# Kernel tuning notes

Hardware: AMD Instinct MI355X
Metric: run time of the kernel (lower is better)

Reference implementation:

```python
import jax, jax.numpy as jnp
import numpy as np

N, NDIM, K, M = 65536, 512, 512, 200


def setup_inputs() -> dict:
    key = jax.random.key(0)
    k1, k2, k3, k4, k5 = jax.random.split(key, 5)
    data = jax.random.normal(k1, (N, NDIM), dtype=jnp.float32)
    # Orthogonal projection A, as in __init__: QR of randn with sign fix
    A0 = np.asarray(jax.random.normal(k2, (NDIM, K), dtype=jnp.float32), dtype=np.float64)
    Q, R = np.linalg.qr(A0)
    A = jnp.asarray(Q * np.sign(np.diag(R)), dtype=jnp.float32)
    # Monotonic knot grids on roughly [-4, 4] with M knots per direction
    span = 8.0 / (M - 1)
    dx = jax.random.uniform(k3, (K, M - 1), minval=0.5 * span, maxval=1.5 * span)
    xx = jnp.concatenate([jnp.full((K, 1), -4.0), -4.0 + jnp.cumsum(dx, axis=1)], axis=1).astype(jnp.float32)
    dy = jax.random.uniform(k4, (K, M - 1), minval=0.5 * span, maxval=1.5 * span)
    yy = jnp.concatenate([jnp.full((K, 1), -4.0), -4.0 + jnp.cumsum(dy, axis=1)], axis=1).astype(jnp.float32)
    delta = jax.random.uniform(k5, (K, M), minval=0.5, maxval=2.0, dtype=jnp.float32)
    return {"data": data, "A": A, "xx": xx, "yy": yy, "delta": delta}


def _rq_spline_forward(x, xx, yy, delta):
    """Monotonic rational-quadratic spline, applied per dimension.
    x: (N, K) values; xx, yy, delta: (K, M) knot positions / values / derivatives.
    Returns (y, log|dy/dx|), both (N, K).
    """
    Mk = xx.shape[1]
    # Per-dimension bin search: idx in [0, Mk]
    idx = jax.vmap(jnp.searchsorted, in_axes=(0, 1))(xx, x).T  # (N, K)
    below = idx == 0
    above = idx == Mk
    b = jnp.clip(idx, 1, Mk - 1) - 1  # interior bin index, (N, K)
    bt = b.T  # (K, N) for take_along_axis on (K, M) tables
    g = lambda t, o: jnp.take_along_axis(t, bt + o, axis=1).T  # -> (N, K)
    xk, xk1 = g(xx, 0), g(xx, 1)
    yk, yk1 = g(yy, 0), g(yy, 1)
    dk, dk1 = g(delta, 0), g(delta, 1)
    dx = xk1 - xk
    dy = yk1 - yk
    s = dy / dx  # bin slope
    xi = jnp.clip((x - xk) / dx, 0.0, 1.0)  # clipped so out-of-range pts stay finite
    xi1 = 1.0 - xi
    denom = s + (dk1 + dk - 2.0 * s) * xi * xi1
    y_in = yk + dy * (s * xi * xi + dk * xi * xi1) / denom
    logd_in = (2.0 * jnp.log(s)
               + jnp.log(dk1 * xi * xi + 2.0 * s * xi * xi1 + dk * xi1 * xi1)
               - 2.0 * jnp.log(denom))
    # Linear extrapolation outside the knot range with endpoint derivatives
    x0, xN_ = xx[:, 0], xx[:, -1]
    y0, yN_ = yy[:, 0], yy[:, -1]
    d0, dN_ = delta[:, 0], delta[:, -1]
    y = jnp.where(below, y0 + d0 * (x - x0),
                  jnp.where(above, yN_ + dN_ * (x - xN_), y_in))
    logd = jnp.where(below, jnp.log(d0),
                     jnp.where(above, jnp.log(dN_), logd_in))
    return y, logd


def reference(data, A, xx, yy, delta):
    data0 = data @ A                    # (N, K) sliced projection
    remaining = data - data0 @ A.T      # component orthogonal to the slices
    y, logd = _rq_spline_forward(data0, xx, yy, delta)
    logj = jnp.sum(logd, axis=1)        # (N,) log-Jacobian
    out = remaining + y @ A.T
    return out, logj
```

## Files before the change

kernel.cpp:

```cpp
#include <hip/hip_runtime.h>

#define N_ROWS 65536
#define DIM 512
#define MKNOTS 200
#define KT 16
#define NCELL 384
#define TILE 256
#define TPB 4

typedef _Float16 f16x8 __attribute__((ext_vector_type(8)));
typedef _Float16 f16x4 __attribute__((ext_vector_type(4)));
typedef float f32x4 __attribute__((ext_vector_type(4)));

__device__ inline void gload16(const void* g, void* l) {
  __builtin_amdgcn_global_load_lds(
      (const __attribute__((address_space(1))) void*)g,
      (__attribute__((address_space(3))) void*)l,
      16, 0, 0);
}

template <bool S3, bool ADDSRC>
__global__ __launch_bounds__(256)
void gemm_k(const _Float16* __restrict__ Ah, const _Float16* __restrict__ Al,
            const _Float16* __restrict__ Bth, const _Float16* __restrict__ Btl,
            const float* __restrict__ addsrc, float* __restrict__ C)
{
  __shared__ alignas(16) _Float16 smem[S3 ? 16384 : 8192];
  _Float16* sAh = smem;
  _Float16* sBh = smem + 4096;
  _Float16* sAl = S3 ? smem + 8192  : smem;
  _Float16* sBl = S3 ? smem + 12288 : smem;

  const int tid  = threadIdx.x;
  const int bm   = blockIdx.x * 128;
  const int bn   = blockIdx.y * 128;
  const int wm   = ((tid >> 6) >> 1) * 64;
  const int wn   = ((tid >> 6) & 1) * 64;
  const int lane = tid & 63;
  const int lm   = lane & 15;
  const int quad = lane >> 4;
  const int sr   = tid >> 2;
  const int sc   = (tid & 3) * 8;

  const _Float16* gAh = Ah  + (size_t)(bm + sr) * DIM + sc;
  const _Float16* gBh = Bth + (size_t)(bn + sr) * DIM + sc;
  const _Float16* gAl = S3 ? (Al  + (size_t)(bm + sr) * DIM + sc) : gAh;
  const _Float16* gBl = S3 ? (Btl + (size_t)(bn + sr) * DIM + sc) : gBh;

  f32x4 acc[4][4] = {};

  for (int k0 = 0; k0 < DIM; k0 += 32) {
    gload16(gAh + k0,               sAh + tid * 8);
    gload16(gAh + k0 + 64 * DIM,    sAh + 2048 + tid * 8);
    gload16(gBh + k0,               sBh + tid * 8);
    gload16(gBh + k0 + 64 * DIM,    sBh + 2048 + tid * 8);
    if constexpr (S3) {
      gload16(gAl + k0,             sAl + tid * 8);
      gload16(gAl + k0 + 64 * DIM,  sAl + 2048 + tid * 8);
      gload16(gBl + k0,             sBl + tid * 8);
      gload16(gBl + k0 + 64 * DIM,  sBl + 2048 + tid * 8);
    }
    __syncthreads();

    f16x8 a_h[4], b_h[4], a_l[4], b_l[4];
    #pragma unroll
    for (int i = 0; i < 4; ++i) {
      a_h[i] = *(const f16x8*)&sAh[(wm + i * 16 + lm) * 32 + quad * 8];
      b_h[i] = *(const f16x8*)&sBh[(wn + i * 16 + lm) * 32 + quad * 8];
      if constexpr (S3) {
        a_l[i] = *(const f16x8*)&sAl[(wm + i * 16 + lm) * 32 + quad * 8];
        b_l[i] = *(const f16x8*)&sBl[(wn + i * 16 + lm) * 32 + quad * 8];
      }
    }
    #pragma unroll
    for (int i = 0; i < 4; ++i)
      #pragma unroll
      for (int j = 0; j < 4; ++j) {
        acc[i][j] = __builtin_amdgcn_mfma_f32_16x16x32_f16(a_h[i], b_h[j], acc[i][j], 0, 0, 0);
        if constexpr (S3) {
          acc[i][j] = __builtin_amdgcn_mfma_f32_16x16x32_f16(a_h[i], b_l[j], acc[i][j], 0, 0, 0);
          acc[i][j] = __builtin_amdgcn_mfma_f32_16x16x32_f16(a_l[i], b_h[j], acc[i][j], 0, 0, 0);
        }
      }
    __syncthreads();
  }

  #pragma unroll
  for (int i = 0; i < 4; ++i)
    #pragma unroll
    for (int j = 0; j < 4; ++j)
      #pragma unroll
      for (int r = 0; r < 4; ++r) {
        const int row = bm + wm + i * 16 + quad * 4 + r;
        const int col = bn + wn + j * 16 + lm;
        const size_t idx = (size_t)row * DIM + col;
        float v = acc[i][j][r];
        if constexpr (ADDSRC) v += addsrc[idx];
        C[idx] = v;
      }
}

__global__ __launch_bounds__(256)
void conv_data_k(const float* __restrict__ in, _Float16* __restrict__ hi,
                 _Float16* __restrict__ lo)
{
  const size_t i = ((size_t)blockIdx.x * 256 + threadIdx.x) * 4;
  const float4 v = *reinterpret_cast<const float4*>(in + i);
  f16x4 h, l;
  h.x = (_Float16)v.x; l.x = (_Float16)(v.x - (float)h.x);
  h.y = (_Float16)v.y; l.y = (_Float16)(v.y - (float)h.y);
  h.z = (_Float16)v.z; l.z = (_Float16)(v.z - (float)h.z);
  h.w = (_Float16)v.w; l.w = (_Float16)(v.w - (float)h.w);
  *reinterpret_cast<f16x4*>(hi + i) = h;
  *reinterpret_cast<f16x4*>(lo + i) = l;
}

__global__ __launch_bounds__(256)
void conv_A_k(const float* __restrict__ A, _Float16* __restrict__ Ah,
              _Float16* __restrict__ Al, _Float16* __restrict__ ATh,
              _Float16* __restrict__ ATl)
{
  const int i = blockIdx.x * 256 + threadIdx.x;
  const int r = i >> 9, c = i & 511;
  const float v = A[i];
  const _Float16 h = (_Float16)v;
  const _Float16 l = (_Float16)(v - (float)h);
  Ah[i] = h; Al[i] = l;
  ATh[c * 512 + r] = h; ATl[c * 512 + r] = l;
}

__global__ __launch_bounds__(256)
void prep_k(const float* __restrict__ xx, const float* __restrict__ yy,
            const float* __restrict__ dd, float4* __restrict__ pkG,
            unsigned char* __restrict__ bucketG)
{
  __shared__ float xr[MKNOTS], yr[MKNOTS];
  const int k = blockIdx.x, tid = threadIdx.x;
  if (tid < MKNOTS) {
    xr[tid] = xx[k * MKNOTS + tid];
    yr[tid] = yy[k * MKNOTS + tid];
  }
  __syncthreads();
  if (tid < MKNOTS) {
    const float x0 = xr[tid], y0 = yr[tid], d0 = dd[k * MKNOTS + tid];
    float s = 0.f;
    if (tid < MKNOTS - 1) s = (yr[tid + 1] - y0) / (xr[tid + 1] - x0);
    pkG[k * MKNOTS + tid] = float4{x0, y0, d0, s};
  }
  for (int c = tid; c < NCELL; c += 256) {
    const float cl = -4.f + (float)c * 0.03125f;
    int lo = 0, hi = MKNOTS;
    while (lo < hi) { const int mid = (lo + hi) >> 1; if (xr[mid] <= cl) lo = mid + 1; else hi = mid; }
    bucketG[k * NCELL + c] = (unsigned char)lo;
  }
}

__global__ __launch_bounds__(256)
void spline_k(const float* __restrict__ data0, const float4* __restrict__ pkG,
              const unsigned char* __restrict__ bucketG,
              _Float16* __restrict__ zH, float* __restrict__ ppart)
{
  __shared__ float sX[KT * 201];
  __shared__ float sY[KT * 201];
  __shared__ _Float16 sD[KT * 201 + 2];
  __shared__ float xT[TILE * 17];

  const int kBase = blockIdx.x * KT;
  const int nBase = blockIdx.y * (TILE * TPB);
  const int tid = threadIdx.x;

  for (int i = tid; i < KT * MKNOTS; i += 256) {
    const int r = i / MKNOTS, c = i - r * MKNOTS;
    const float4 v = pkG[(kBase + r) * MKNOTS + c];
    sX[r * 201 + c] = v.x;
    sY[r * 201 + c] = v.y;
    sD[r * 201 + c] = (_Float16)v.z;
  }
  __syncthreads();

  for (int tile = 0; tile < TPB; ++tile) {
    const int n0 = nBase + tile * TILE;

    #pragma unroll
    for (int rr = 0; rr < 4; ++rr) {
      const int r = rr * 64 + (tid >> 2);
      const float4 v = *((const float4*)(data0 + (size_t)(n0 + r) * DIM + kBase) + (tid & 3));
      float* dst = &xT[r * 17 + (tid & 3) * 4];
      dst[0] = v.x; dst[1] = v.y; dst[2] = v.z; dst[3] = v.w;
    }
    __syncthreads();

    float acc = 0.f;
    float zprev = 0.f;
    #pragma unroll 4
    for (int j = 0; j < KT; ++j) {
      const float x = xT[tid * 17 + j];

      int c = (int)((x + 4.f) * 32.f);
      c = min(max(c, 0), NCELL - 1);
      const int cnt0 = (int)bucketG[(kBase + j) * NCELL + c];

      const int p = min(cnt0, MKNOTS - 2);
      const int q0 = p - 1;
      const float* rx = &sX[j * 201];
      const float xm = rx[q0], x0 = rx[q0 + 1], x1 = rx[q0 + 2], x2 = rx[q0 + 3];
      const int t2 = (x0 < x ? 1 : 0) + (x1 < x ? 1 : 0);
      const int idx = p + t2;
      const bool below = (x <= -4.f);
      const bool above = (idx >= MKNOTS);
      const int b = idx - 1;

      const float xk  = (t2 == 0) ? xm : ((t2 == 1) ? x0 : x1);
      const float xk1 = (t2 == 0) ? x0 : ((t2 == 1) ? x1 : x2);
      const float yk  = sY[j * 201 + b];
      const float yk1 = sY[j * 201 + b + 1];
      const float dk  = (float)sD[j * 201 + b];
      const float dk1 = (float)sD[j * 201 + b + 1];

      const float dxk = xk1 - xk;
      const float rdx = __builtin_amdgcn_rcpf(dxk);
      const float s   = (yk1 - yk) * rdx;
      float xi = (x - xk) * rdx;
      xi = fminf(fmaxf(xi, 0.f), 1.f);
      const float xi1 = 1.f - xi;
      const float g = xi * xi1;
      const float den = s + (dk1 + dk - 2.f * s) * g;
      const float rden = __builtin_amdgcn_rcpf(den);
      const float y_in = yk + s * dxk * (s * xi * xi + dk * g) * rden;
      const float dnum = dk1 * xi * xi + 2.f * s * g + dk * xi1 * xi1;
      const float ld_in = __logf(s * s * dnum * rden * rden);

      const bool edge = below || above;
      const float y  = edge ? (yk + dk * (x - xk)) : y_in;
      const float ld = edge ? __logf(dk) : ld_in;
      acc += ld;

      const float z = y - x;
      if (j & 1) {
        union { _Float16 h[2]; unsigned int u; } pk2;
        pk2.h[0] = (_Float16)zprev; pk2.h[1] = (_Float16)z;
        ((unsigned int*)xT)[tid * 17 + (j >> 1)] = pk2.u;
      } else {
        zprev = z;
      }
    }
    ppart[(size_t)blockIdx.x * N_ROWS + n0 + tid] = acc;
    __syncthreads();

    const int w = tid & 7;
    #pragma unroll
    for (int ri = 0; ri < 8; ++ri) {
      const int r = ri * 32 + (tid >> 3);
      const unsigned int zz = ((const unsigned int*)xT)[r * 17 + w];
      *(unsigned int*)(zH + (size_t)(n0 + r) * DIM + kBase + w * 2) = zz;
    }
    __syncthreads();
  }
}

__global__ __launch_bounds__(256)
void reduce_k(const float* __restrict__ ppart, float* __restrict__ logj)
{
  const int n = blockIdx.x * 256 + threadIdx.x;
  float a = 0.f;
  #pragma unroll
  for (int t = 0; t < 32; ++t) a += ppart[(size_t)t * N_ROWS + n];
  logj[n] = a;
}

extern "C" void kernel_launch(void* const* d_in, const int* in_sizes, int n_in,
                              void* d_out, int out_size, void* d_ws, size_t ws_size,
                              hipStream_t stream)
{
  const float* data  = (const float*)d_in[0];
  const float* A     = (const float*)d_in[1];
  const float* xx    = (const float*)d_in[2];
  const float* yy    = (const float*)d_in[3];
  const float* delta = (const float*)d_in[4];

  float* out  = (float*)d_out;
  float* logj = out + (size_t)N_ROWS * DIM;

  _Float16* dHi = (_Float16*)d_ws;
  _Float16* dLo = dHi + (size_t)N_ROWS * DIM;
  _Float16* Ah  = dLo + (size_t)N_ROWS * DIM;
  _Float16* Al  = Ah + 512 * 512;
  _Float16* ATh = Al + 512 * 512;
  _Float16* ATl = ATh + 512 * 512;
  float* data0  = (float*)(ATl + 512 * 512);
  _Float16* zH  = dHi;
  float4* pkG = (float4*)dLo;
  unsigned char* bucketG = (unsigned char*)(pkG + 512 * MKNOTS);
  float* ppart = (float*)(bucketG + 512 * NCELL);

  conv_A_k<<<1024, 256, 0, stream>>>(A, Ah, Al, ATh, ATl);
  conv_data_k<<<(N_ROWS * DIM) / (256 * 4), 256, 0, stream>>>(data, dHi, dLo);

  gemm_k<true, false><<<dim3(N_ROWS / 128, DIM / 128), 256, 0, stream>>>(
      dHi, dLo, ATh, ATl, nullptr, data0);

  prep_k<<<512, 256, 0, stream>>>(xx, yy, delta, pkG, bucketG);

  spline_k<<<dim3(DIM / KT, N_ROWS / (TILE * TPB)), 256, 0, stream>>>(
      data0, pkG, bucketG, zH, ppart);

  reduce_k<<<N_ROWS / 256, 256, 0, stream>>>(ppart, logj);

  gemm_k<false, true><<<dim3(N_ROWS / 128, DIM / 128), 256, 0, stream>>>(
      zH, nullptr, Ah, nullptr, data, out);
}
```

Baseline: 601.6 us.

## Restructure spline kernel: packed float4 knot table, finer buckets, register-staged rows

The spline kernel now holds each knot as a packed float4 (x, y, delta, 1/dx) in LDS and uses a finer bucket grid (768 cells, 8 dims per block). That cuts the bin search to a single comparison and replaces the per-bin divide with a precomputed reciprocal. Each thread reads its own row's 8 inputs straight from global memory with prefetch, and writes 16-byte z vectors directly, removing the LDS transpose and barriers. The trade-off is uncoalesced strided row access, more blocks, and more partial sums for reduce_k to combine. It also sets an occupancy hint of 5 waves.

```diff
diff --git a/kernel.cpp b/kernel.cpp
--- a/kernel.cpp
+++ b/kernel.cpp
@@ -3,14 +3,16 @@
 #define N_ROWS 65536
 #define DIM 512
 #define MKNOTS 200
-#define KT 16
-#define NCELL 384
+#define KT 8
+#define NCELL 768
 #define TILE 256
 #define TPB 4
+#define NKT (DIM / KT)
 
 typedef _Float16 f16x8 __attribute__((ext_vector_type(8)));
 typedef _Float16 f16x4 __attribute__((ext_vector_type(4)));
 typedef float f32x4 __attribute__((ext_vector_type(4)));
+typedef unsigned int u32x4 __attribute__((ext_vector_type(4)));
 
 __device__ inline void gload16(const void* g, void* l) {
   __builtin_amdgcn_global_load_lds(
@@ -134,36 +136,32 @@
             const float* __restrict__ dd, float4* __restrict__ pkG,
             unsigned char* __restrict__ bucketG)
 {
-  __shared__ float xr[MKNOTS], yr[MKNOTS];
+  __shared__ float xr[MKNOTS];
   const int k = blockIdx.x, tid = threadIdx.x;
-  if (tid < MKNOTS) {
-    xr[tid] = xx[k * MKNOTS + tid];
-    yr[tid] = yy[k * MKNOTS + tid];
-  }
+  if (tid < MKNOTS) xr[tid] = xx[k * MKNOTS + tid];
   __syncthreads();
   if (tid < MKNOTS) {
-    const float x0 = xr[tid], y0 = yr[tid], d0 = dd[k * MKNOTS + tid];
-    float s = 0.f;
-    if (tid < MKNOTS - 1) s = (yr[tid + 1] - y0) / (xr[tid + 1] - x0);
-    pkG[k * MKNOTS + tid] = float4{x0, y0, d0, s};
+    const float x0 = xr[tid];
+    const float y0 = yy[k * MKNOTS + tid];
+    const float d0 = dd[k * MKNOTS + tid];
+    float rdx = 0.f;
+    if (tid < MKNOTS - 1) rdx = 1.0f / (xr[tid + 1] - x0);
+    pkG[k * MKNOTS + tid] = float4{x0, y0, d0, rdx};
   }
   for (int c = tid; c < NCELL; c += 256) {
-    const float cl = -4.f + (float)c * 0.03125f;
+    const float cl = -4.f + (float)c * 0.015625f;
     int lo = 0, hi = MKNOTS;
     while (lo < hi) { const int mid = (lo + hi) >> 1; if (xr[mid] <= cl) lo = mid + 1; else hi = mid; }
     bucketG[k * NCELL + c] = (unsigned char)lo;
   }
 }
 
-__global__ __launch_bounds__(256)
+__global__ __launch_bounds__(256, 5)
 void spline_k(const float* __restrict__ data0, const float4* __restrict__ pkG,
               const unsigned char* __restrict__ bucketG,
               _Float16* __restrict__ zH, float* __restrict__ ppart)
 {
-  __shared__ float sX[KT * 201];
-  __shared__ float sY[KT * 201];
-  __shared__ _Float16 sD[KT * 201 + 2];
-  __shared__ float xT[TILE * 17];
+  __shared__ float4 pkL[KT * 201];
 
   const int kBase = blockIdx.x * KT;
   const int nBase = blockIdx.y * (TILE * TPB);
@@ -171,90 +169,74 @@
 
   for (int i = tid; i < KT * MKNOTS; i += 256) {
     const int r = i / MKNOTS, c = i - r * MKNOTS;
-    const float4 v = pkG[(kBase + r) * MKNOTS + c];
-    sX[r * 201 + c] = v.x;
-    sY[r * 201 + c] = v.y;
-    sD[r * 201 + c] = (_Float16)v.z;
-  }
+    pkL[r * 201 + c] = pkG[(kBase + r) * MKNOTS + c];
+  }
+  if (tid < KT) pkL[tid * 201 + 200] = float4{0.f, 0.f, 0.f, 0.f};
   __syncthreads();
 
-  for (int tile = 0; tile < TPB; ++tile) {
-    const int n0 = nBase + tile * TILE;
-
-    #pragma unroll
-    for (int rr = 0; rr < 4; ++rr) {
-      const int r = rr * 64 + (tid >> 2);
-      const float4 v = *((const float4*)(data0 + (size_t)(n0 + r) * DIM + kBase) + (tid & 3));
-      float* dst = &xT[r * 17 + (tid & 3) * 4];
-      dst[0] = v.x; dst[1] = v.y; dst[2] = v.z; dst[3] = v.w;
-    }
-    __syncthreads();
+  const unsigned char* bRow = bucketG + (size_t)kBase * NCELL;
+  const float* xp0 = data0 + (size_t)(nBase + tid) * DIM + kBase;
+
+  float4 v0 = *(const float4*)xp0;
+  float4 v1 = *(const float4*)(xp0 + 4);
+
+  #pragma unroll
+  for (int t = 0; t < TPB; ++t) {
+    const float x8[8] = {v0.x, v0.y, v0.z, v0.w, v1.x, v1.y, v1.z, v1.w};
+    if (t + 1 < TPB) {
+      const float* xp = xp0 + (size_t)(t + 1) * TILE * DIM;
+      v0 = *(const float4*)xp;
+      v1 = *(const float4*)(xp + 4);
+    }
 
     float acc = 0.f;
     float zprev = 0.f;
-    #pragma unroll 4
+    unsigned int zw[4];
+    #pragma unroll
     for (int j = 0; j < KT; ++j) {
-      const float x = xT[tid * 17 + j];
-
-      int c = (int)((x + 4.f) * 32.f);
+      const float x = x8[j];
+
+      int c = (int)(x * 64.f + 256.f);
       c = min(max(c, 0), NCELL - 1);
-      const int cnt0 = (int)bucketG[(kBase + j) * NCELL + c];
-
-      const int p = min(cnt0, MKNOTS - 2);
-      const int q0 = p - 1;
-      const float* rx = &sX[j * 201];
-      const float xm = rx[q0], x0 = rx[q0 + 1], x1 = rx[q0 + 2], x2 = rx[q0 + 3];
-      const int t2 = (x0 < x ? 1 : 0) + (x1 < x ? 1 : 0);
-      const int idx = p + t2;
-      const bool below = (x <= -4.f);
-      const bool above = (idx >= MKNOTS);
-      const int b = idx - 1;
-
-      const float xk  = (t2 == 0) ? xm : ((t2 == 1) ? x0 : x1);
-      const float xk1 = (t2 == 0) ? x0 : ((t2 == 1) ? x1 : x2);
-      const float yk  = sY[j * 201 + b];
-      const float yk1 = sY[j * 201 + b + 1];
-      const float dk  = (float)sD[j * 201 + b];
-      const float dk1 = (float)sD[j * 201 + b + 1];
-
-      const float dxk = xk1 - xk;
-      const float rdx = __builtin_amdgcn_rcpf(dxk);
-      const float s   = (yk1 - yk) * rdx;
-      float xi = (x - xk) * rdx;
+      const int cnt = (int)bRow[j * NCELL + c];
+      const int q = min(cnt, MKNOTS - 1);
+      const float xq = pkL[j * 201 + q].x;
+      const int b = min(cnt + (xq < x ? 1 : 0), MKNOTS) - 1;
+
+      const float4 p0 = pkL[j * 201 + b];
+      const float4 p1 = pkL[j * 201 + b + 1];
+
+      const float dy = p1.y - p0.y;
+      const float s  = dy * p0.w;
+      float xi = (x - p0.x) * p0.w;
       xi = fminf(fmaxf(xi, 0.f), 1.f);
       const float xi1 = 1.f - xi;
       const float g = xi * xi1;
-      const float den = s + (dk1 + dk - 2.f * s) * g;
+      const float den = s + (p1.z + p0.z - 2.f * s) * g;
       const float rden = __builtin_amdgcn_rcpf(den);
-      const float y_in = yk + s * dxk * (s * xi * xi + dk * g) * rden;
-      const float dnum = dk1 * xi * xi + 2.f * s * g + dk * xi1 * xi1;
-      const float ld_in = __logf(s * s * dnum * rden * rden);
-
-      const bool edge = below || above;
-      const float y  = edge ? (yk + dk * (x - xk)) : y_in;
-      const float ld = edge ? __logf(dk) : ld_in;
-      acc += ld;
+      const float y_in = p0.y + dy * (s * xi * xi + p0.z * g) * rden;
+      const float dnum = p1.z * xi * xi + 2.f * s * g + p0.z * xi1 * xi1;
+
+      const bool edge = (x <= -4.f) || (b == MKNOTS - 1);
+      const float larg = edge ? p0.z : (s * s * dnum) * (rden * rden);
+      acc += __logf(larg);
+      const float y = edge ? (p0.y + p0.z * (x - p0.x)) : y_in;
 
       const float z = y - x;
       if (j & 1) {
         union { _Float16 h[2]; unsigned int u; } pk2;
         pk2.h[0] = (_Float16)zprev; pk2.h[1] = (_Float16)z;
-        ((unsigned int*)xT)[tid * 17 + (j >> 1)] = pk2.u;
+        zw[j >> 1] = pk2.u;
       } else {
         zprev = z;
       }
     }
-    ppart[(size_t)blockIdx.x * N_ROWS + n0 + tid] = acc;
-    __syncthreads();
-
-    const int w = tid & 7;
-    #pragma unroll
-    for (int ri = 0; ri < 8; ++ri) {
-      const int r = ri * 32 + (tid >> 3);
-      const unsigned int zz = ((const unsigned int*)xT)[r * 17 + w];
-      *(unsigned int*)(zH + (size_t)(n0 + r) * DIM + kBase + w * 2) = zz;
-    }
-    __syncthreads();
+
+    const int row = nBase + t * TILE + tid;
+    ppart[(size_t)blockIdx.x * N_ROWS + row] = acc;
+    union { unsigned int w[4]; u32x4 v4; } zu;
+    zu.w[0] = zw[0]; zu.w[1] = zw[1]; zu.w[2] = zw[2]; zu.w[3] = zw[3];
+    *(u32x4*)(zH + (size_t)row * DIM + kBase) = zu.v4;
   }
 }
 
@@ -264,7 +246,7 @@
   const int n = blockIdx.x * 256 + threadIdx.x;
   float a = 0.f;
   #pragma unroll
-  for (int t = 0; t < 32; ++t) a += ppart[(size_t)t * N_ROWS + n];
+  for (int t = 0; t < NKT; ++t) a += ppart[(size_t)t * N_ROWS + n];
   logj[n] = a;
 }
 
```

New measurement: 665.3 us. +10.6%, slower.
